# Kernel tuning notes

Measured on AMD Instinct MI355X. Metric: run time of the kernel, lower is better.

Reference implementation:

```python
import jax, jax.numpy as jnp
import numpy as np

DIM = 1024
HEADS = 16
B, N = 2, 2048


def setup_inputs() -> dict:
    key = jax.random.key(0)
    ks = jax.random.split(key, 10)
    s = 1.0 / np.sqrt(DIM)
    return {
        "y2_for": jax.random.normal(ks[0], (B, N, DIM), jnp.float32),
        "y2_back": jax.random.normal(ks[1], (B, N, DIM), jnp.float32),
        "Wq": jax.random.normal(ks[2], (DIM, DIM), jnp.float32) * s,
        "bq": jnp.zeros((DIM,), jnp.float32),
        "Wk": jax.random.normal(ks[3], (DIM, DIM), jnp.float32) * s,
        "bk": jnp.zeros((DIM,), jnp.float32),
        "Wv": jax.random.normal(ks[4], (DIM, DIM), jnp.float32) * s,
        "bv": jnp.zeros((DIM,), jnp.float32),
        "Wo": jax.random.normal(ks[5], (DIM, DIM), jnp.float32) * s,
        "bo": jnp.zeros((DIM,), jnp.float32),
    }


def reference(y2_for, y2_back, Wq, bq, Wk, bk, Wv, bv, Wo, bo):
    h = HEADS
    d = DIM // h
    scale = d ** -0.5
    q = y2_for @ Wq + bq                    # [b, n, dim]
    k = y2_back @ Wk + bk
    v = (y2_back + y2_for) @ Wv + bv

    def split_heads(x):
        b, n, _ = x.shape
        return x.reshape(b, n, h, d).transpose(0, 2, 1, 3)  # [b, h, n, d]

    q, k, v = split_heads(q), split_heads(k), split_heads(v)
    attn = jax.nn.softmax(jnp.einsum('bhid,bhjd->bhij', q, k) * scale, axis=-1)
    out = jnp.einsum('bhij,bhjd->bhid', attn, v)
    out = out.transpose(0, 2, 1, 3).reshape(y2_for.shape)   # [b, n, dim]
    out = out + y2_for + y2_back
    return out @ Wo + bo
```

## Files before the change

### kernel.cpp

```cpp
#include <hip/hip_runtime.h>

#define DIM 1024
#define HEADS 16
#define BB 2
#define NN 2048
#define HD 64
#define M_ROWS (BB*NN)

typedef __bf16 bf16x8 __attribute__((ext_vector_type(8)));
typedef float f32x4 __attribute__((ext_vector_type(4)));
typedef short s16x4 __attribute__((ext_vector_type(4)));

__device__ inline unsigned short f2bf(float f) {
    unsigned int u = __builtin_bit_cast(unsigned int, f);
    u += 0x7fffu + ((u >> 16) & 1u);
    return (unsigned short)(u >> 16);
}
__device__ inline float bf2f(unsigned short u) {
    return __builtin_bit_cast(float, (unsigned int)u << 16);
}
__device__ inline bf16x8 as_bf16x8(uint4 v) {
    return __builtin_bit_cast(bf16x8, v);
}
__device__ __forceinline__ void gl_lds16(const unsigned short* g, unsigned short* l) {
    __builtin_amdgcn_global_load_lds(
        (const __attribute__((address_space(1))) unsigned int*)g,
        (__attribute__((address_space(3))) unsigned int*)l, 16, 0, 0);
}

__device__ __forceinline__ f32x4 mfma16x16x16bf16(s16x4 a, s16x4 b, f32x4 c) {
#if __has_builtin(__builtin_amdgcn_mfma_f32_16x16x16bf16_1k)
    return __builtin_amdgcn_mfma_f32_16x16x16bf16_1k(a, b, c, 0, 0, 0);
#else
    asm volatile("v_mfma_f32_16x16x16_bf16 %0, %1, %2, %0"
                 : "+v"(c) : "v"(a), "v"(b));
    return c;
#endif
}

__global__ __launch_bounds__(256) void prep_w(
    const float* __restrict__ Wq, const float* __restrict__ Wk,
    const float* __restrict__ Wv, const float* __restrict__ Wo,
    unsigned short* __restrict__ Wt_all)
{
    __shared__ float tile[32][33];
    const int m = blockIdx.z;
    const float* W = (m == 0) ? Wq : (m == 1) ? Wk : (m == 2) ? Wv : Wo;
    const int bk = blockIdx.x, bn = blockIdx.y;
    const int tx = threadIdx.x & 31, ty = threadIdx.x >> 5;

    #pragma unroll
    for (int i = 0; i < 32; i += 8)
        tile[ty + i][tx] = W[(size_t)(bk*32 + ty + i)*DIM + bn*32 + tx];
    __syncthreads();
    unsigned short* dst = Wt_all + (size_t)m * DIM * DIM;
    #pragma unroll
    for (int i = 0; i < 32; i += 8)
        dst[(size_t)(bn*32 + ty + i)*DIM + bk*32 + tx] = f2bf(tile[tx][ty + i]);
}

__global__ __launch_bounds__(256) void prep_act(
    const float* __restrict__ y2f, const float* __restrict__ y2b,
    unsigned short* __restrict__ Af, unsigned short* __restrict__ Ab,
    unsigned short* __restrict__ As)
{
    const size_t idx = ((size_t)blockIdx.x*256 + threadIdx.x) * 8;
    #pragma unroll
    for (int half = 0; half < 2; half++) {
        float4 f = *(const float4*)(y2f + idx + half*4);
        float4 b = *(const float4*)(y2b + idx + half*4);
        ushort4 of, ob, os;
        of.x = f2bf(f.x); of.y = f2bf(f.y); of.z = f2bf(f.z); of.w = f2bf(f.w);
        ob.x = f2bf(b.x); ob.y = f2bf(b.y); ob.z = f2bf(b.z); ob.w = f2bf(b.w);
        os.x = f2bf(f.x + b.x); os.y = f2bf(f.y + b.y);
        os.z = f2bf(f.z + b.z); os.w = f2bf(f.w + b.w);
        *(ushort4*)(Af + idx + half*4) = of;
        *(ushort4*)(Ab + idx + half*4) = ob;
        *(ushort4*)(As + idx + half*4) = os;
    }
}

__global__ __launch_bounds__(256) void gemm_qkv(
    const unsigned short* __restrict__ Af, const unsigned short* __restrict__ Ab,
    const unsigned short* __restrict__ As,
    const unsigned short* __restrict__ Wt_all,
    const float* __restrict__ bq, const float* __restrict__ bk,
    const float* __restrict__ bv,
    unsigned short* __restrict__ Qh, unsigned short* __restrict__ Kh,
    unsigned short* __restrict__ Vt)
{
    const int bm = blockIdx.x;
    const int mode = blockIdx.y >> 3;
    const int bn = blockIdx.y & 7;
    __shared__ __align__(16) unsigned short smem[16384];
    const int t = threadIdx.x;
    const int w = t >> 6, lane = t & 63, ln = lane & 15, quad = lane >> 4;
    const int wm = w >> 1, wn = w & 1;
    const unsigned short* Wt = Wt_all + (size_t)mode * (DIM*DIM);
    const unsigned short* A0 = (mode == 0) ? Af : (mode == 1) ? Ab : As;

    const int srow = lane >> 2;
    const int scol = (lane & 3) * 8;

    f32x4 acc[4][4];
    #pragma unroll
    for (int mi = 0; mi < 4; mi++)
        #pragma unroll
        for (int ni = 0; ni < 4; ni++)
            acc[mi][ni] = (f32x4){0.f, 0.f, 0.f, 0.f};

#define STAGE_G(KT, BUF) do { \
        unsigned short* sa_ = smem + (BUF)*8192; \
        _Pragma("unroll") \
        for (int j = 0; j < 2; j++) { \
            int row = w*32 + j*16; \
            gl_lds16(A0 + (size_t)(bm*128 + row + srow)*DIM + (KT)*32 + scol, \
                     &sa_[row*32]); \
            gl_lds16(Wt + (size_t)(bn*128 + row + srow)*DIM + (KT)*32 + scol, \
                     &sa_[4096 + row*32]); \
        } } while (0)

    STAGE_G(0, 0);
    asm volatile("s_waitcnt vmcnt(0)" ::: "memory");
    __builtin_amdgcn_s_barrier();
    __builtin_amdgcn_sched_barrier(0);

    #pragma unroll 2
    for (int kt = 0; kt < 32; kt++) {
        const int cur = kt & 1;
        if (kt < 31) STAGE_G(kt + 1, cur ^ 1);

        const unsigned short* sa = smem + cur*8192;
        const unsigned short* sb = sa + 4096;
        bf16x8 af[4], bfr[4];
        #pragma unroll
        for (int mi = 0; mi < 4; mi++)
            af[mi] = as_bf16x8(*(const uint4*)(&sa[(wm*64 + mi*16 + ln)*32 + quad*8]));
        #pragma unroll
        for (int ni = 0; ni < 4; ni++)
            bfr[ni] = as_bf16x8(*(const uint4*)(&sb[(wn*64 + ni*16 + ln)*32 + quad*8]));
        #pragma unroll
        for (int mi = 0; mi < 4; mi++)
            #pragma unroll
            for (int ni = 0; ni < 4; ni++)
                acc[mi][ni] = __builtin_amdgcn_mfma_f32_16x16x32_bf16(af[mi], bfr[ni], acc[mi][ni], 0, 0, 0);

        __builtin_amdgcn_sched_barrier(0);
        if (kt < 31) {
            asm volatile("s_waitcnt vmcnt(0)" ::: "memory");
            __builtin_amdgcn_s_barrier();
            __builtin_amdgcn_sched_barrier(0);
        }
    }
#undef STAGE_G

    const float* bias = (mode == 0) ? bq : (mode == 1) ? bk : bv;
    unsigned short* dst = (mode == 0) ? Qh : (mode == 1) ? Kh : Vt;
    if (mode < 2) {
        const float sc = (mode == 0) ? 0.125f * 1.4426950408889634f : 1.0f;
        #pragma unroll
        for (int mi = 0; mi < 4; mi++) {
            #pragma unroll
            for (int r = 0; r < 4; r++) {
                int grow = bm*128 + wm*64 + mi*16 + quad*4 + r;
                int b_ = grow >> 11, n = grow & (NN - 1);
                #pragma unroll
                for (int ni = 0; ni < 4; ni++) {
                    int gcol = bn*128 + wn*64 + ni*16 + ln;
                    int hh = gcol >> 6, dd = gcol & 63;
                    float val = (acc[mi][ni][r] + bias[gcol]) * sc;
                    dst[(((size_t)(b_*HEADS + hh))*NN + n)*HD + dd] = f2bf(val);
                }
            }
        }
    } else {
        __syncthreads();
        #pragma unroll
        for (int ni = 0; ni < 4; ni++) {
            int row_s = wn*64 + ni*16 + ln;
            float bsv = bias[bn*128 + row_s];
            int sxor = (row_s & 7) << 1;
            #pragma unroll
            for (int mi = 0; mi < 4; mi++) {
                int u = wm*16 + mi*4 + quad;
                ushort4 pk;
                pk.x = f2bf(acc[mi][ni][0] + bsv);
                pk.y = f2bf(acc[mi][ni][1] + bsv);
                pk.z = f2bf(acc[mi][ni][2] + bsv);
                pk.w = f2bf(acc[mi][ni][3] + bsv);
                *(ushort4*)(&smem[row_s*128 + ((u ^ sxor) << 2)]) = pk;
            }
        }
        __syncthreads();
        const int b_ = bm >> 4;
        #pragma unroll
        for (int i = 0; i < 8; i++) {
            int idx = i*256 + t;
            int dd = idx >> 4, jc = idx & 15;
            int u = (jc*2) ^ ((dd & 7) << 1);
            int hh = bn*2 + (dd >> 6), d_ = dd & 63;
            *(uint4*)(dst + (((size_t)(b_*HEADS + hh))*HD + d_)*NN
                          + (size_t)(bm & 15)*128 + jc*8)
                = *(const uint4*)(&smem[dd*128 + (u << 2)]);
        }
    }
}

__global__ __launch_bounds__(256) void gemm_out(
    const unsigned short* __restrict__ attp,
    const unsigned short* __restrict__ Wt_all,
    const float* __restrict__ bo, float* __restrict__ out)
{
    const int bm = blockIdx.x, bn = blockIdx.y;
    __shared__ __align__(16) unsigned short smem[12288];
    const int t = threadIdx.x;
    const int w = t >> 6, lane = t & 63, ln = lane & 15, quad = lane >> 4;
    const int wm = w >> 1, wn = w & 1;
    const unsigned short* Wt = Wt_all + (size_t)3 * (DIM*DIM);

    const int srow = lane >> 2;
    const int scol = (lane & 3) * 8;

    f32x4 acc[2][4];
    #pragma unroll
    for (int mi = 0; mi < 2; mi++)
        #pragma unroll
        for (int ni = 0; ni < 4; ni++)
            acc[mi][ni] = (f32x4){0.f, 0.f, 0.f, 0.f};

#define STAGE_O(KT, BUF) do { \
        unsigned short* sa_ = smem + (BUF)*6144; \
        gl_lds16(attp + (size_t)(bm*64 + w*16 + srow)*DIM + (KT)*32 + scol, \
                 &sa_[(w*16)*32]); \
        _Pragma("unroll") \
        for (int j = 0; j < 2; j++) { \
            int row = w*32 + j*16; \
            gl_lds16(Wt + (size_t)(bn*128 + row + srow)*DIM + (KT)*32 + scol, \
                     &sa_[2048 + row*32]); \
        } } while (0)

    STAGE_O(0, 0);
    asm volatile("s_waitcnt vmcnt(0)" ::: "memory");
    __builtin_amdgcn_s_barrier();
    __builtin_amdgcn_sched_barrier(0);

    #pragma unroll 2
    for (int kt = 0; kt < 32; kt++) {
        const int cur = kt & 1;
        if (kt < 31) STAGE_O(kt + 1, cur ^ 1);

        const unsigned short* sa = smem + cur*6144;
        const unsigned short* sb = sa + 2048;
        bf16x8 af[2], bfr[4];
        #pragma unroll
        for (int mi = 0; mi < 2; mi++)
            af[mi] = as_bf16x8(*(const uint4*)(&sa[(wm*32 + mi*16 + ln)*32 + quad*8]));
        #pragma unroll
        for (int ni = 0; ni < 4; ni++)
            bfr[ni] = as_bf16x8(*(const uint4*)(&sb[(wn*64 + ni*16 + ln)*32 + quad*8]));
        #pragma unroll
        for (int mi = 0; mi < 2; mi++)
            #pragma unroll
            for (int ni = 0; ni < 4; ni++)
                acc[mi][ni] = __builtin_amdgcn_mfma_f32_16x16x32_bf16(af[mi], bfr[ni], acc[mi][ni], 0, 0, 0);

        __builtin_amdgcn_sched_barrier(0);
        if (kt < 31) {
            asm volatile("s_waitcnt vmcnt(0)" ::: "memory");
            __builtin_amdgcn_s_barrier();
            __builtin_amdgcn_sched_barrier(0);
        }
    }
#undef STAGE_O

    #pragma unroll
    for (int mi = 0; mi < 2; mi++) {
        #pragma unroll
        for (int r = 0; r < 4; r++) {
            int grow = bm*64 + wm*32 + mi*16 + quad*4 + r;
            #pragma unroll
            for (int ni = 0; ni < 4; ni++) {
                int gcol = bn*128 + wn*64 + ni*16 + ln;
                out[(size_t)grow*DIM + gcol] = acc[mi][ni][r] + bo[gcol];
            }
        }
    }
}

__global__ __launch_bounds__(256) void attn_kernel(
    const unsigned short* __restrict__ Qh, const unsigned short* __restrict__ Kh,
    const unsigned short* __restrict__ Vt, const unsigned short* __restrict__ As,
    unsigned short* __restrict__ attp)
{
    const int bh = blockIdx.x;
    const int qt = blockIdx.y;
    const int b = bh >> 4, h = bh & 15;
    const int t = threadIdx.x;
    const int w = t >> 6, lane = t & 63, ln = lane & 15, quad = lane >> 4;
    const int sw = ln & 7;
    const float EBIAS = 17.312340490667562f;

    __shared__ __align__(16) unsigned short sK[2][64*64];
    __shared__ __align__(16) unsigned short sVt[2][64*64];

    const unsigned short* Qb  = Qh + (size_t)bh * NN * HD + (size_t)qt * 64 * HD;
    const unsigned short* Kb  = Kh + (size_t)bh * NN * HD;
    const unsigned short* Vtb = Vt + (size_t)bh * HD * NN;

    const int rl = lane >> 3, cb = lane & 7;

    bf16x8 aq[2];
    #pragma unroll
    for (int k = 0; k < 2; k++)
        aq[k] = as_bf16x8(*(const uint4*)(Qb + (size_t)(w*16 + ln)*HD + (k*4 + quad)*8));

#define STAGE_KV(JT, BBUF) do { \
        _Pragma("unroll") \
        for (int j = 0; j < 2; j++) { \
            int row = w*16 + j*8 + rl; \
            gl_lds16(Kb + (size_t)((JT)*64 + row)*HD + ((cb ^ (row & 7))*8), \
                     &sK[BBUF][(w*16 + j*8)*64]); \
            gl_lds16(Vtb + (size_t)row*NN + (JT)*64 + ((cb ^ (row & 7))*8), \
                     &sVt[BBUF][(w*16 + j*8)*64]); \
        } } while (0)

    const s16x4 ones = { (short)0x3F80, (short)0x3F80, (short)0x3F80, (short)0x3F80 };
    f32x4 accO[4], accL;
    accL = (f32x4){0.f, 0.f, 0.f, 0.f};
    #pragma unroll
    for (int di = 0; di < 4; di++) accO[di] = (f32x4){0.f, 0.f, 0.f, 0.f};

    STAGE_KV(0, 0);
    asm volatile("s_waitcnt vmcnt(0)" ::: "memory");
    __builtin_amdgcn_s_barrier();
    __builtin_amdgcn_sched_barrier(0);

    #pragma unroll 2
    for (int jt = 0; jt < 32; jt++) {
        const int cur = jt & 1;
        if (jt < 31) STAGE_KV(jt + 1, cur ^ 1);

        const unsigned short* sKc = sK[cur];
        const unsigned short* sVc = sVt[cur];

        f32x4 accS[4];
        #pragma unroll
        for (int ni = 0; ni < 4; ni++)
            accS[ni] = (f32x4){-EBIAS, -EBIAS, -EBIAS, -EBIAS};
        __builtin_amdgcn_s_setprio(1);
        #pragma unroll
        for (int ni = 0; ni < 4; ni++)
            #pragma unroll
            for (int k = 0; k < 2; k++) {
                bf16x8 bkf = as_bf16x8(*(const uint4*)(
                    &sKc[(ni*16 + ln)*64 + (((k*4 + quad) ^ sw)*8)]));
                accS[ni] = __builtin_amdgcn_mfma_f32_16x16x32_bf16(bkf, aq[k], accS[ni], 0, 0, 0);
            }
        __builtin_amdgcn_s_setprio(0);

        s16x4 pf[4];
        #pragma unroll
        for (int ni = 0; ni < 4; ni++) {
            unsigned int e0 = __builtin_bit_cast(unsigned int, __builtin_amdgcn_exp2f(accS[ni][0]));
            unsigned int e1 = __builtin_bit_cast(unsigned int, __builtin_amdgcn_exp2f(accS[ni][1]));
            unsigned int e2 = __builtin_bit_cast(unsigned int, __builtin_amdgcn_exp2f(accS[ni][2]));
            unsigned int e3 = __builtin_bit_cast(unsigned int, __builtin_amdgcn_exp2f(accS[ni][3]));
            unsigned int lo = __builtin_amdgcn_perm(e1, e0, 0x07060302u);
            unsigned int hi = __builtin_amdgcn_perm(e3, e2, 0x07060302u);
            pf[ni] = __builtin_bit_cast(s16x4, uint2{lo, hi});
            accL = mfma16x16x16bf16(pf[ni], ones, accL);
        }

        __builtin_amdgcn_s_setprio(1);
        #pragma unroll
        for (int ni = 0; ni < 4; ni++) {
            int blkv = 2*ni + (quad >> 1);
            int off = (quad & 1) * 4;
            #pragma unroll
            for (int di = 0; di < 4; di++) {
                s16x4 bv = __builtin_bit_cast(s16x4,
                    *(const uint2*)(&sVc[(di*16 + ln)*64 + ((blkv ^ sw)*8) + off]));
                accO[di] = mfma16x16x16bf16(pf[ni], bv, accO[di]);
            }
        }
        __builtin_amdgcn_s_setprio(0);

        __builtin_amdgcn_sched_barrier(0);
        if (jt < 31) {
            asm volatile("s_waitcnt vmcnt(0)" ::: "memory");
            __builtin_amdgcn_s_barrier();
            __builtin_amdgcn_sched_barrier(0);
        }
    }
#undef STAGE_KV

    #pragma unroll
    for (int r = 0; r < 4; r++) {
        float inv = 1.f / accL[r];
        int n = qt*64 + w*16 + quad*4 + r;
        #pragma unroll
        for (int di = 0; di < 4; di++) {
            int c = h*64 + di*16 + ln;
            size_t gi = ((size_t)b*NN + n)*DIM + c;
            float o = accO[di][r]*inv + bf2f(As[gi]);
            attp[gi] = f2bf(o);
        }
    }
}

extern "C" void kernel_launch(void* const* d_in, const int* in_sizes, int n_in,
                              void* d_out, int out_size, void* d_ws, size_t ws_size,
                              hipStream_t stream) {
    const float* y2f = (const float*)d_in[0];
    const float* y2b = (const float*)d_in[1];
    const float* Wq  = (const float*)d_in[2];
    const float* bq  = (const float*)d_in[3];
    const float* Wk  = (const float*)d_in[4];
    const float* bk  = (const float*)d_in[5];
    const float* Wv  = (const float*)d_in[6];
    const float* bv  = (const float*)d_in[7];
    const float* Wo  = (const float*)d_in[8];
    const float* bo  = (const float*)d_in[9];
    float* out = (float*)d_out;

    const size_t NACT = (size_t)M_ROWS * DIM;
    unsigned short* ws   = (unsigned short*)d_ws;
    unsigned short* Af   = ws;
    unsigned short* Ab   = ws + NACT;
    unsigned short* As   = ws + 2*NACT;
    unsigned short* Qh   = ws + 3*NACT;
    unsigned short* Kh   = ws + 4*NACT;
    unsigned short* Vt   = ws + 5*NACT;
    unsigned short* Wt   = ws + 6*NACT;
    unsigned short* attp = Ab;

    prep_w<<<dim3(32, 32, 4), 256, 0, stream>>>(Wq, Wk, Wv, Wo, Wt);
    prep_act<<<dim3(2048), 256, 0, stream>>>(y2f, y2b, Af, Ab, As);
    gemm_qkv<<<dim3(32, 24), 256, 0, stream>>>(
        Af, Ab, As, Wt, bq, bk, bv, Qh, Kh, Vt);
    attn_kernel<<<dim3(32, 32), 256, 0, stream>>>(Qh, Kh, Vt, As, attp);
    gemm_out<<<dim3(64, 8), 256, 0, stream>>>(attp, Wt, bo, out);
}
```

Measured before the change: 227.4 us.

## Triple-buffer GEMM loads, precompute LDS pointers, merge prep kernels

```diff
diff --git a/kernel.cpp b/kernel.cpp
--- a/kernel.cpp
+++ b/kernel.cpp
@@ -38,45 +38,42 @@
 #endif
 }
 
-__global__ __launch_bounds__(256) void prep_w(
+__global__ __launch_bounds__(256) void prep_all(
+    const float* __restrict__ y2f, const float* __restrict__ y2b,
     const float* __restrict__ Wq, const float* __restrict__ Wk,
     const float* __restrict__ Wv, const float* __restrict__ Wo,
-    unsigned short* __restrict__ Wt_all)
+    unsigned short* __restrict__ Af, unsigned short* __restrict__ Ab,
+    unsigned short* __restrict__ As, unsigned short* __restrict__ Wt_all)
 {
     __shared__ float tile[32][33];
-    const int m = blockIdx.z;
-    const float* W = (m == 0) ? Wq : (m == 1) ? Wk : (m == 2) ? Wv : Wo;
-    const int bk = blockIdx.x, bn = blockIdx.y;
-    const int tx = threadIdx.x & 31, ty = threadIdx.x >> 5;
-
-    #pragma unroll
-    for (int i = 0; i < 32; i += 8)
-        tile[ty + i][tx] = W[(size_t)(bk*32 + ty + i)*DIM + bn*32 + tx];
-    __syncthreads();
-    unsigned short* dst = Wt_all + (size_t)m * DIM * DIM;
-    #pragma unroll
-    for (int i = 0; i < 32; i += 8)
-        dst[(size_t)(bn*32 + ty + i)*DIM + bk*32 + tx] = f2bf(tile[tx][ty + i]);
-}
-
-__global__ __launch_bounds__(256) void prep_act(
-    const float* __restrict__ y2f, const float* __restrict__ y2b,
-    unsigned short* __restrict__ Af, unsigned short* __restrict__ Ab,
-    unsigned short* __restrict__ As)
-{
-    const size_t idx = ((size_t)blockIdx.x*256 + threadIdx.x) * 8;
-    #pragma unroll
-    for (int half = 0; half < 2; half++) {
-        float4 f = *(const float4*)(y2f + idx + half*4);
-        float4 b = *(const float4*)(y2b + idx + half*4);
-        ushort4 of, ob, os;
-        of.x = f2bf(f.x); of.y = f2bf(f.y); of.z = f2bf(f.z); of.w = f2bf(f.w);
-        ob.x = f2bf(b.x); ob.y = f2bf(b.y); ob.z = f2bf(b.z); ob.w = f2bf(b.w);
-        os.x = f2bf(f.x + b.x); os.y = f2bf(f.y + b.y);
-        os.z = f2bf(f.z + b.z); os.w = f2bf(f.w + b.w);
-        *(ushort4*)(Af + idx + half*4) = of;
-        *(ushort4*)(Ab + idx + half*4) = ob;
-        *(ushort4*)(As + idx + half*4) = os;
+    const int blk = blockIdx.x;
+    if (blk < 4096) {
+        const int m = blk >> 10, r = blk & 1023, bk = r & 31, bn = r >> 5;
+        const float* W = (m == 0) ? Wq : (m == 1) ? Wk : (m == 2) ? Wv : Wo;
+        const int tx = threadIdx.x & 31, ty = threadIdx.x >> 5;
+        #pragma unroll
+        for (int i = 0; i < 32; i += 8)
+            tile[ty + i][tx] = W[(size_t)(bk*32 + ty + i)*DIM + bn*32 + tx];
+        __syncthreads();
+        unsigned short* dst = Wt_all + (size_t)m * DIM * DIM;
+        #pragma unroll
+        for (int i = 0; i < 32; i += 8)
+            dst[(size_t)(bn*32 + ty + i)*DIM + bk*32 + tx] = f2bf(tile[tx][ty + i]);
+    } else {
+        const size_t idx = ((size_t)(blk - 4096)*256 + threadIdx.x) * 8;
+        #pragma unroll
+        for (int half = 0; half < 2; half++) {
+            float4 f = *(const float4*)(y2f + idx + half*4);
+            float4 b = *(const float4*)(y2b + idx + half*4);
+            ushort4 of, ob, os;
+            of.x = f2bf(f.x); of.y = f2bf(f.y); of.z = f2bf(f.z); of.w = f2bf(f.w);
+            ob.x = f2bf(b.x); ob.y = f2bf(b.y); ob.z = f2bf(b.z); ob.w = f2bf(b.w);
+            os.x = f2bf(f.x + b.x); os.y = f2bf(f.y + b.y);
+            os.z = f2bf(f.z + b.z); os.w = f2bf(f.w + b.w);
+            *(ushort4*)(Af + idx + half*4) = of;
+            *(ushort4*)(Ab + idx + half*4) = ob;
+            *(ushort4*)(As + idx + half*4) = os;
+        }
     }
 }
 
@@ -92,7 +89,7 @@
     const int bm = blockIdx.x;
     const int mode = blockIdx.y >> 3;
     const int bn = blockIdx.y & 7;
-    __shared__ __align__(16) unsigned short smem[16384];
+    __shared__ __align__(16) unsigned short smem[3*8192];
     const int t = threadIdx.x;
     const int w = t >> 6, lane = t & 63, ln = lane & 15, quad = lane >> 4;
     const int wm = w >> 1, wn = w & 1;
@@ -102,6 +99,14 @@
     const int srow = lane >> 2;
     const int scol = (lane & 3) * 8;
 
+    const unsigned short* gA0 = A0 + (size_t)(bm*128 + w*32 + srow)*DIM + scol;
+    const unsigned short* gA1 = gA0 + (size_t)16*DIM;
+    const unsigned short* gB0 = Wt + (size_t)(bn*128 + w*32 + srow)*DIM + scol;
+    const unsigned short* gB1 = gB0 + (size_t)16*DIM;
+
+    const int aoff = (wm*64 + ln)*32 + quad*8;
+    const int boff = 4096 + (wn*64 + ln)*32 + quad*8;
+
     f32x4 acc[4][4];
     #pragma unroll
     for (int mi = 0; mi < 4; mi++)
@@ -109,50 +114,56 @@
         for (int ni = 0; ni < 4; ni++)
             acc[mi][ni] = (f32x4){0.f, 0.f, 0.f, 0.f};
 
-#define STAGE_G(KT, BUF) do { \
-        unsigned short* sa_ = smem + (BUF)*8192; \
-        _Pragma("unroll") \
-        for (int j = 0; j < 2; j++) { \
-            int row = w*32 + j*16; \
-            gl_lds16(A0 + (size_t)(bm*128 + row + srow)*DIM + (KT)*32 + scol, \
-                     &sa_[row*32]); \
-            gl_lds16(Wt + (size_t)(bn*128 + row + srow)*DIM + (KT)*32 + scol, \
-                     &sa_[4096 + row*32]); \
-        } } while (0)
-
-    STAGE_G(0, 0);
+#define STAGE_Q(BUF) do { \
+        unsigned short* s_ = smem + (BUF)*8192; \
+        gl_lds16(gA0, &s_[(w*32)*32]); \
+        gl_lds16(gA1, &s_[(w*32 + 16)*32]); \
+        gl_lds16(gB0, &s_[4096 + (w*32)*32]); \
+        gl_lds16(gB1, &s_[4096 + (w*32 + 16)*32]); \
+        gA0 += 32; gA1 += 32; gB0 += 32; gB1 += 32; } while (0)
+
+#define COMP_Q(BUF) do { \
+        const unsigned short* s_ = smem + (BUF)*8192; \
+        bf16x8 af[4], bfr[4]; \
+        _Pragma("unroll") \
+        for (int mi = 0; mi < 4; mi++) \
+            af[mi] = as_bf16x8(*(const uint4*)(s_ + aoff + mi*512)); \
+        _Pragma("unroll") \
+        for (int ni = 0; ni < 4; ni++) \
+            bfr[ni] = as_bf16x8(*(const uint4*)(s_ + boff + ni*512)); \
+        _Pragma("unroll") \
+        for (int mi = 0; mi < 4; mi++) \
+            _Pragma("unroll") \
+            for (int ni = 0; ni < 4; ni++) \
+                acc[mi][ni] = __builtin_amdgcn_mfma_f32_16x16x32_bf16(af[mi], bfr[ni], acc[mi][ni], 0, 0, 0); \
+    } while (0)
+
+#define QITER(B) do { \
+        asm volatile("s_waitcnt vmcnt(4)" ::: "memory"); \
+        __builtin_amdgcn_s_barrier(); \
+        __builtin_amdgcn_sched_barrier(0); \
+        STAGE_Q(((B) + 2) % 3); \
+        COMP_Q(B); \
+        __builtin_amdgcn_sched_barrier(0); \
+    } while (0)
+
+    STAGE_Q(0);
+    STAGE_Q(1);
+    for (int base = 0; base < 30; base += 3) {
+        QITER(0); QITER(1); QITER(2);
+    }
+    asm volatile("s_waitcnt vmcnt(4)" ::: "memory");
+    __builtin_amdgcn_s_barrier();
+    __builtin_amdgcn_sched_barrier(0);
+    COMP_Q(0);
+    __builtin_amdgcn_sched_barrier(0);
     asm volatile("s_waitcnt vmcnt(0)" ::: "memory");
     __builtin_amdgcn_s_barrier();
     __builtin_amdgcn_sched_barrier(0);
-
-    #pragma unroll 2
-    for (int kt = 0; kt < 32; kt++) {
-        const int cur = kt & 1;
-        if (kt < 31) STAGE_G(kt + 1, cur ^ 1);
-
-        const unsigned short* sa = smem + cur*8192;
-        const unsigned short* sb = sa + 4096;
-        bf16x8 af[4], bfr[4];
-        #pragma unroll
-        for (int mi = 0; mi < 4; mi++)
-            af[mi] = as_bf16x8(*(const uint4*)(&sa[(wm*64 + mi*16 + ln)*32 + quad*8]));
-        #pragma unroll
-        for (int ni = 0; ni < 4; ni++)
-            bfr[ni] = as_bf16x8(*(const uint4*)(&sb[(wn*64 + ni*16 + ln)*32 + quad*8]));
-        #pragma unroll
-        for (int mi = 0; mi < 4; mi++)
-            #pragma unroll
-            for (int ni = 0; ni < 4; ni++)
-                acc[mi][ni] = __builtin_amdgcn_mfma_f32_16x16x32_bf16(af[mi], bfr[ni], acc[mi][ni], 0, 0, 0);
-
-        __builtin_amdgcn_sched_barrier(0);
-        if (kt < 31) {
-            asm volatile("s_waitcnt vmcnt(0)" ::: "memory");
-            __builtin_amdgcn_s_barrier();
-            __builtin_amdgcn_sched_barrier(0);
-        }
-    }
-#undef STAGE_G
+    COMP_Q(1);
+#undef QITER
+#undef COMP_Q
+#undef STAGE_Q
 
     const float* bias = (mode == 0) ? bq : (mode == 1) ? bk : bv;
     unsigned short* dst = (mode == 0) ? Qh : (mode == 1) ? Kh : Vt;
@@ -212,7 +223,7 @@
     const float* __restrict__ bo, float* __restrict__ out)
 {
     const int bm = blockIdx.x, bn = blockIdx.y;
-    __shared__ __align__(16) unsigned short smem[12288];
+    __shared__ __align__(16) unsigned short smem[3*6144];
     const int t = threadIdx.x;
     const int w = t >> 6, lane = t & 63, ln = lane & 15, quad = lane >> 4;
     const int wm = w >> 1, wn = w & 1;
@@ -221,6 +232,13 @@
     const int srow = lane >> 2;
     const int scol = (lane & 3) * 8;
 
+    const unsigned short* gA = attp + (size_t)(bm*64 + w*16 + srow)*DIM + scol;
+    const unsigned short* gB0 = Wt + (size_t)(bn*128 + w*32 + srow)*DIM + scol;
+    const unsigned short* gB1 = gB0 + (size_t)16*DIM;
+
+    const int aoff = (wm*32 + ln)*32 + quad*8;
+    const int boff = 2048 + (wn*64 + ln)*32 + quad*8;
+
     f32x4 acc[2][4];
     #pragma unroll
     for (int mi = 0; mi < 2; mi++)
@@ -228,50 +246,55 @@
         for (int ni = 0; ni < 4; ni++)
             acc[mi][ni] = (f32x4){0.f, 0.f, 0.f, 0.f};
 
-#define STAGE_O(KT, BUF) do { \
-        unsigned short* sa_ = smem + (BUF)*6144; \
-        gl_lds16(attp + (size_t)(bm*64 + w*16 + srow)*DIM + (KT)*32 + scol, \
-                 &sa_[(w*16)*32]); \
-        _Pragma("unroll") \
-        for (int j = 0; j < 2; j++) { \
-            int row = w*32 + j*16; \
-            gl_lds16(Wt + (size_t)(bn*128 + row + srow)*DIM + (KT)*32 + scol, \
-                     &sa_[2048 + row*32]); \
-        } } while (0)
-
-    STAGE_O(0, 0);
+#define STAGE_T(BUF) do { \
+        unsigned short* s_ = smem + (BUF)*6144; \
+        gl_lds16(gA, &s_[(w*16)*32]); \
+        gl_lds16(gB0, &s_[2048 + (w*32)*32]); \
+        gl_lds16(gB1, &s_[2048 + (w*32 + 16)*32]); \
+        gA += 32; gB0 += 32; gB1 += 32; } while (0)
+
+#define COMP_T(BUF) do { \
+        const unsigned short* s_ = smem + (BUF)*6144; \
+        bf16x8 af[2], bfr[4]; \
+        _Pragma("unroll") \
+        for (int mi = 0; mi < 2; mi++) \
+            af[mi] = as_bf16x8(*(const uint4*)(s_ + aoff + mi*512)); \
+        _Pragma("unroll") \
+        for (int ni = 0; ni < 4; ni++) \
+            bfr[ni] = as_bf16x8(*(const uint4*)(s_ + boff + ni*512)); \
+        _Pragma("unroll") \
+        for (int mi = 0; mi < 2; mi++) \
+            _Pragma("unroll") \
+            for (int ni = 0; ni < 4; ni++) \
+                acc[mi][ni] = __builtin_amdgcn_mfma_f32_16x16x32_bf16(af[mi], bfr[ni], acc[mi][ni], 0, 0, 0); \
+    } while (0)
+
+#define TITER(B) do { \
+        asm volatile("s_waitcnt vmcnt(3)" ::: "memory"); \
+        __builtin_amdgcn_s_barrier(); \
+        __builtin_amdgcn_sched_barrier(0); \
+        STAGE_T(((B) + 2) % 3); \
+        COMP_T(B); \
+        __builtin_amdgcn_sched_barrier(0); \
+    } while (0)
+
+    STAGE_T(0);
+    STAGE_T(1);
+    for (int base = 0; base < 30; base += 3) {
+        TITER(0); TITER(1); TITER(2);
+    }
+    asm volatile("s_waitcnt vmcnt(3)" ::: "memory");
+    __builtin_amdgcn_s_barrier();
+    __builtin_amdgcn_sched_barrier(0);
+    COMP_T(0);
+    __builtin_amdgcn_sched_barrier(0);
     asm volatile("s_waitcnt vmcnt(0)" ::: "memory");
     __builtin_amdgcn_s_barrier();
     __builtin_amdgcn_sched_barrier(0);
-
-    #pragma unroll 2
-    for (int kt = 0; kt < 32; kt++) {
-        const int cur = kt & 1;
-        if (kt < 31) STAGE_O(kt + 1, cur ^ 1);
-
-        const unsigned short* sa = smem + cur*6144;
-        const unsigned short* sb = sa + 2048;
-        bf16x8 af[2], bfr[4];
-        #pragma unroll
-        for (int mi = 0; mi < 2; mi++)
-            af[mi] = as_bf16x8(*(const uint4*)(&sa[(wm*32 + mi*16 + ln)*32 + quad*8]));
-        #pragma unroll
-        for (int ni = 0; ni < 4; ni++)
-            bfr[ni] = as_bf16x8(*(const uint4*)(&sb[(wn*64 + ni*16 + ln)*32 + quad*8]));
-        #pragma unroll
-        for (int mi = 0; mi < 2; mi++)
-            #pragma unroll
-            for (int ni = 0; ni < 4; ni++)
-                acc[mi][ni] = __builtin_amdgcn_mfma_f32_16x16x32_bf16(af[mi], bfr[ni], acc[mi][ni], 0, 0, 0);
-
-        __builtin_amdgcn_sched_barrier(0);
-        if (kt < 31) {
-            asm volatile("s_waitcnt vmcnt(0)" ::: "memory");
-            __builtin_amdgcn_s_barrier();
-            __builtin_amdgcn_sched_barrier(0);
-        }
-    }
-#undef STAGE_O
+    COMP_T(1);
+#undef TITER
+#undef COMP_T
+#undef STAGE_T
 
     #pragma unroll
     for (int mi = 0; mi < 2; mi++) {
@@ -314,15 +337,34 @@
     for (int k = 0; k < 2; k++)
         aq[k] = as_bf16x8(*(const uint4*)(Qb + (size_t)(w*16 + ln)*HD + (k*4 + quad)*8));
 
-#define STAGE_KV(JT, BBUF) do { \
-        _Pragma("unroll") \
-        for (int j = 0; j < 2; j++) { \
-            int row = w*16 + j*8 + rl; \
-            gl_lds16(Kb + (size_t)((JT)*64 + row)*HD + ((cb ^ (row & 7))*8), \
-                     &sK[BBUF][(w*16 + j*8)*64]); \
-            gl_lds16(Vtb + (size_t)row*NN + (JT)*64 + ((cb ^ (row & 7))*8), \
-                     &sVt[BBUF][(w*16 + j*8)*64]); \
-        } } while (0)
+    const int r0 = w*16 + rl, r1 = w*16 + 8 + rl;
+    const unsigned short* gK0 = Kb + (size_t)r0*HD + (cb ^ (r0 & 7))*8;
+    const unsigned short* gK1 = Kb + (size_t)r1*HD + (cb ^ (r1 & 7))*8;
+    const unsigned short* gV0 = Vtb + (size_t)r0*NN + (cb ^ (r0 & 7))*8;
+    const unsigned short* gV1 = Vtb + (size_t)r1*NN + (cb ^ (r1 & 7))*8;
+
+#define STAGE_KV(BUF) do { \
+        gl_lds16(gK0, &sK[BUF][(w*16)*64]); \
+        gl_lds16(gK1, &sK[BUF][(w*16 + 8)*64]); \
+        gl_lds16(gV0, &sVt[BUF][(w*16)*64]); \
+        gl_lds16(gV1, &sVt[BUF][(w*16 + 8)*64]); \
+        gK0 += 64*HD; gK1 += 64*HD; gV0 += 64; gV1 += 64; } while (0)
+
+    const int kc0 = ((quad ^ (sw & 3)) + 4*((sw >> 2) & 1)) * 8;
+    const unsigned short* bK0a = &sK[0][ln*64 + kc0];
+    const unsigned short* bK0b = &sK[0][ln*64 + (kc0 ^ 32)];
+    const unsigned short* bK1a = &sK[1][ln*64 + kc0];
+    const unsigned short* bK1b = &sK[1][ln*64 + (kc0 ^ 32)];
+    const int vb = ln*64 + ((quad >> 1) ^ (sw & 1))*8 + (quad & 1)*4;
+    const int sv = (sw >> 1) & 3;
+    const unsigned short* bV0_0 = &sVt[0][vb + (0 ^ sv)*16];
+    const unsigned short* bV0_1 = &sVt[0][vb + (1 ^ sv)*16];
+    const unsigned short* bV0_2 = &sVt[0][vb + (2 ^ sv)*16];
+    const unsigned short* bV0_3 = &sVt[0][vb + (3 ^ sv)*16];
+    const unsigned short* bV1_0 = &sVt[1][vb + (0 ^ sv)*16];
+    const unsigned short* bV1_1 = &sVt[1][vb + (1 ^ sv)*16];
+    const unsigned short* bV1_2 = &sVt[1][vb + (2 ^ sv)*16];
+    const unsigned short* bV1_3 = &sVt[1][vb + (3 ^ sv)*16];
 
     const s16x4 ones = { (short)0x3F80, (short)0x3F80, (short)0x3F80, (short)0x3F80 };
     f32x4 accO[4], accL;
@@ -330,68 +372,68 @@
     #pragma unroll
     for (int di = 0; di < 4; di++) accO[di] = (f32x4){0.f, 0.f, 0.f, 0.f};
 
-    STAGE_KV(0, 0);
-    asm volatile("s_waitcnt vmcnt(0)" ::: "memory");
-    __builtin_amdgcn_s_barrier();
-    __builtin_amdgcn_sched_barrier(0);
-
-    #pragma unroll 2
-    for (int jt = 0; jt < 32; jt++) {
-        const int cur = jt & 1;
-        if (jt < 31) STAGE_KV(jt + 1, cur ^ 1);
-
-        const unsigned short* sKc = sK[cur];
-        const unsigned short* sVc = sVt[cur];
-
-        f32x4 accS[4];
-        #pragma unroll
-        for (int ni = 0; ni < 4; ni++)
-            accS[ni] = (f32x4){-EBIAS, -EBIAS, -EBIAS, -EBIAS};
-        __builtin_amdgcn_s_setprio(1);
-        #pragma unroll
-        for (int ni = 0; ni < 4; ni++)
-            #pragma unroll
-            for (int k = 0; k < 2; k++) {
-                bf16x8 bkf = as_bf16x8(*(const uint4*)(
-                    &sKc[(ni*16 + ln)*64 + (((k*4 + quad) ^ sw)*8)]));
-                accS[ni] = __builtin_amdgcn_mfma_f32_16x16x32_bf16(bkf, aq[k], accS[ni], 0, 0, 0);
-            }
-        __builtin_amdgcn_s_setprio(0);
-
-        s16x4 pf[4];
-        #pragma unroll
-        for (int ni = 0; ni < 4; ni++) {
-            unsigned int e0 = __builtin_bit_cast(unsigned int, __builtin_amdgcn_exp2f(accS[ni][0]));
-            unsigned int e1 = __builtin_bit_cast(unsigned int, __builtin_amdgcn_exp2f(accS[ni][1]));
-            unsigned int e2 = __builtin_bit_cast(unsigned int, __builtin_amdgcn_exp2f(accS[ni][2]));
-            unsigned int e3 = __builtin_bit_cast(unsigned int, __builtin_amdgcn_exp2f(accS[ni][3]));
-            unsigned int lo = __builtin_amdgcn_perm(e1, e0, 0x07060302u);
-            unsigned int hi = __builtin_amdgcn_perm(e3, e2, 0x07060302u);
-            pf[ni] = __builtin_bit_cast(s16x4, uint2{lo, hi});
-            accL = mfma16x16x16bf16(pf[ni], ones, accL);
-        }
-
-        __builtin_amdgcn_s_setprio(1);
-        #pragma unroll
-        for (int ni = 0; ni < 4; ni++) {
-            int blkv = 2*ni + (quad >> 1);
-            int off = (quad & 1) * 4;
-            #pragma unroll
-            for (int di = 0; di < 4; di++) {
-                s16x4 bv = __builtin_bit_cast(s16x4,
-                    *(const uint2*)(&sVc[(di*16 + ln)*64 + ((blkv ^ sw)*8) + off]));
-                accO[di] = mfma16x16x16bf16(pf[ni], bv, accO[di]);
-            }
-        }
-        __builtin_amdgcn_s_setprio(0);
-
-        __builtin_amdgcn_sched_barrier(0);
-        if (jt < 31) {
-            asm volatile("s_waitcnt vmcnt(0)" ::: "memory");
-            __builtin_amdgcn_s_barrier();
-            __builtin_amdgcn_sched_barrier(0);
-        }
-    }
+#define ATT_JT(PK0_, PK1_, PV0_, PV1_, PV2_, PV3_) do { \
+        f32x4 accS[4]; \
+        _Pragma("unroll") \
+        for (int ni = 0; ni < 4; ni++) \
+            accS[ni] = (f32x4){-EBIAS, -EBIAS, -EBIAS, -EBIAS}; \
+        __builtin_amdgcn_s_setprio(1); \
+        _Pragma("unroll") \
+        for (int ni = 0; ni < 4; ni++) { \
+            bf16x8 b0_ = as_bf16x8(*(const uint4*)(PK0_ + ni*1024)); \
+            accS[ni] = __builtin_amdgcn_mfma_f32_16x16x32_bf16(b0_, aq[0], accS[ni], 0, 0, 0); \
+            bf16x8 b1_ = as_bf16x8(*(const uint4*)(PK1_ + ni*1024)); \
+            accS[ni] = __builtin_amdgcn_mfma_f32_16x16x32_bf16(b1_, aq[1], accS[ni], 0, 0, 0); \
+        } \
+        __builtin_amdgcn_s_setprio(0); \
+        s16x4 pf[4]; \
+        _Pragma("unroll") \
+        for (int ni = 0; ni < 4; ni++) { \
+            unsigned int e0 = __builtin_bit_cast(unsigned int, __builtin_amdgcn_exp2f(accS[ni][0])); \
+            unsigned int e1 = __builtin_bit_cast(unsigned int, __builtin_amdgcn_exp2f(accS[ni][1])); \
+            unsigned int e2 = __builtin_bit_cast(unsigned int, __builtin_amdgcn_exp2f(accS[ni][2])); \
+            unsigned int e3 = __builtin_bit_cast(unsigned int, __builtin_amdgcn_exp2f(accS[ni][3])); \
+            unsigned int lo = __builtin_amdgcn_perm(e1, e0, 0x07060302u); \
+            unsigned int hi = __builtin_amdgcn_perm(e3, e2, 0x07060302u); \
+            pf[ni] = __builtin_bit_cast(s16x4, uint2{lo, hi}); \
+            accL = mfma16x16x16bf16(pf[ni], ones, accL); \
+        } \
+        __builtin_amdgcn_s_setprio(1); \
+        _Pragma("unroll") \
+        for (int ni = 0; ni < 4; ni++) { \
+            const unsigned short* pv_ = (ni == 0) ? PV0_ : (ni == 1) ? PV1_ \
+                                      : (ni == 2) ? PV2_ : PV3_; \
+            _Pragma("unroll") \
+            for (int di = 0; di < 4; di++) \
+                accO[di] = mfma16x16x16bf16(pf[ni], \
+                    __builtin_bit_cast(s16x4, *(const uint2*)(pv_ + di*1024)), accO[di]); \
+        } \
+        __builtin_amdgcn_s_setprio(0); \
+    } while (0)
+
+#define ATT_SYNC() do { \
+        __builtin_amdgcn_sched_barrier(0); \
+        asm volatile("s_waitcnt vmcnt(0)" ::: "memory"); \
+        __builtin_amdgcn_s_barrier(); \
+        __builtin_amdgcn_sched_barrier(0); \
+    } while (0)
+
+    STAGE_KV(0);
+    ATT_SYNC();
+    for (int jt2 = 0; jt2 < 15; jt2++) {
+        STAGE_KV(1);
+        ATT_JT(bK0a, bK0b, bV0_0, bV0_1, bV0_2, bV0_3);
+        ATT_SYNC();
+        STAGE_KV(0);
+        ATT_JT(bK1a, bK1b, bV1_0, bV1_1, bV1_2, bV1_3);
+        ATT_SYNC();
+    }
+    STAGE_KV(1);
+    ATT_JT(bK0a, bK0b, bV0_0, bV0_1, bV0_2, bV0_3);
+    ATT_SYNC();
+    ATT_JT(bK1a, bK1b, bV1_0, bV1_1, bV1_2, bV1_3);
+#undef ATT_SYNC
+#undef ATT_JT
 #undef STAGE_KV
 
     #pragma unroll
@@ -434,8 +476,8 @@
     unsigned short* Wt   = ws + 6*NACT;
     unsigned short* attp = Ab;
 
-    prep_w<<<dim3(32, 32, 4), 256, 0, stream>>>(Wq, Wk, Wv, Wo, Wt);
-    prep_act<<<dim3(2048), 256, 0, stream>>>(y2f, y2b, Af, Ab, As);
+    prep_all<<<dim3(6144), 256, 0, stream>>>(y2f, y2b, Wq, Wk, Wv, Wo,
+                                             Af, Ab, As, Wt);
     gemm_qkv<<<dim3(32, 24), 256, 0, stream>>>(
         Af, Ab, As, Wt, bq, bk, bv, Qh, Kh, Vt);
     attn_kernel<<<dim3(32, 32), 256, 0, stream>>>(Qh, Kh, Vt, As, attp);
```

Result: faster. 218.8 us (-3.8%).
